# Performance work log

Hardware: AMD Instinct MI355X
Metric: run time of the kernel (lower is better)

The kernel has to match this reference:

```python
import jax, jax.numpy as jnp
import numpy as np

N_NODES = 100000
N_EDGES = 1600000
HIDDEN = 48
LAYERS = 4
ALPHA = 0.1
THETA = 0.5


def setup_inputs() -> dict:
    key = jax.random.key(0)
    ks = jax.random.split(key, 6)
    x = jax.random.normal(ks[0], (N_NODES, 3), dtype=jnp.float32)
    edge_index = jax.random.randint(ks[1], (2, N_EDGES), 0, N_NODES, dtype=jnp.int32)
    W0 = jax.random.normal(ks[2], (3, HIDDEN), dtype=jnp.float32) * 0.3
    b0 = jnp.zeros((HIDDEN,), dtype=jnp.float32)
    convW = jax.random.normal(ks[3], (LAYERS, HIDDEN, HIDDEN), dtype=jnp.float32) * (1.0 / np.sqrt(HIDDEN))
    W1 = jax.random.normal(ks[4], (HIDDEN, HIDDEN), dtype=jnp.float32) * (1.0 / np.sqrt(HIDDEN))
    b1 = jnp.zeros((HIDDEN,), dtype=jnp.float32)
    return {"x": x, "edge_index": edge_index, "W0": W0, "b0": b0,
            "convW": convW, "W1": W1, "b1": b1}


def reference(x, edge_index, W0, b0, convW, W1, b1):
    # lin0 + relu; x0 is the initial residual (dropout=0 / eval mode -> identity)
    h = jax.nn.relu(x @ W0 + b0)
    x0 = h
    src, dst = edge_index[0], edge_index[1]
    n = h.shape[0]
    for l in range(LAYERS):
        # sparse propagation: A @ h via gather + segment_sum (unit edge weights, normalize=False)
        agg = jax.ops.segment_sum(h[src], dst, num_segments=n)
        beta = float(np.log(THETA / (l + 1) + 1.0))
        # GCNII shared-weights branch: t = (1-alpha)*Ah + alpha*x0; out = (1-beta)*t + beta*(t @ W)
        t = (1.0 - ALPHA) * agg + ALPHA * x0
        h = jax.nn.relu((1.0 - beta) * t + beta * (t @ convW[l]))
    out = h @ W1 + b1
    return jax.nn.log_softmax(out, axis=-1)
```

## Files before the change

### kernel.cpp

```cpp
#include <hip/hip_runtime.h>
#include <math.h>

#define N_NODES 100000
#define N_EDGES 1600000
#define HID 48
#define HPAD 64
#define ALPHA 0.1f

#define LBLK 6250
#define NPW 4

typedef unsigned short u16;
typedef unsigned int u32;

__device__ __forceinline__ float bf_lo(u32 u) { return __uint_as_float(u << 16); }
__device__ __forceinline__ float bf_hi(u32 u) { return __uint_as_float(u & 0xffff0000u); }
__device__ __forceinline__ u16 f2bf(float f) {
    u32 b = __float_as_uint(f);
    b += 0x7fff + ((b >> 16) & 1);
    return (u16)(b >> 16);
}
__device__ __forceinline__ u32 pack2(float a, float b) {
    return (u32)f2bf(a) | ((u32)f2bf(b) << 16);
}

#define RLANE(x, l) __int_as_float(__builtin_amdgcn_readlane(__float_as_int(x), (l)))

__global__ __launch_bounds__(256) void lin0_k(const float* __restrict__ x, const float* __restrict__ W0,
                                              const float* __restrict__ b0, u16* __restrict__ h0) {
    int t = blockIdx.x * 256 + threadIdx.x;
    if (t >= N_NODES * 6) return;
    int node = t / 6, oct = t % 6;
    float xv0 = x[node * 3 + 0], xv1 = x[node * 3 + 1], xv2 = x[node * 3 + 2];
    float v[8];
#pragma unroll
    for (int j = 0; j < 8; j++) {
        int f = oct * 8 + j;
        float s = b0[f] + xv0 * W0[0 * HID + f] + xv1 * W0[1 * HID + f] + xv2 * W0[2 * HID + f];
        v[j] = s > 0.f ? s : 0.f;
    }
    uint4 p;
    p.x = pack2(v[0], v[1]); p.y = pack2(v[2], v[3]);
    p.z = pack2(v[4], v[5]); p.w = pack2(v[6], v[7]);
    *(uint4*)(h0 + (size_t)node * HPAD + oct * 8) = p;
}

__global__ __launch_bounds__(256) void count_k(const int* __restrict__ dst, int* __restrict__ deg,
                                               int* __restrict__ rank) {
    int e = blockIdx.x * 256 + threadIdx.x;
    if (e < N_EDGES) rank[e] = atomicAdd(&deg[dst[e]], 1);
}

__global__ __launch_bounds__(256) void scan1_k(const int* __restrict__ deg, int* __restrict__ rowptr,
                                               int* __restrict__ partial) {
    __shared__ int sums[256];
    int tid = threadIdx.x;
    int base = blockIdx.x * 2048 + tid * 8;
    int v[8]; int s = 0;
#pragma unroll
    for (int j = 0; j < 8; j++) { int idx = base + j; v[j] = (idx < N_NODES) ? deg[idx] : 0; s += v[j]; }
    sums[tid] = s; __syncthreads();
    for (int off = 1; off < 256; off <<= 1) {
        int t = (tid >= off) ? sums[tid - off] : 0;
        __syncthreads();
        sums[tid] += t;
        __syncthreads();
    }
    if (tid == 255) partial[blockIdx.x] = sums[255];
    int run = (tid > 0) ? sums[tid - 1] : 0;
#pragma unroll
    for (int j = 0; j < 8; j++) { int idx = base + j; if (idx < N_NODES) rowptr[idx] = run; run += v[j]; }
}

__global__ void scan2_k(int* __restrict__ partial, int* __restrict__ rowptr, int nblk) {
    int lane = threadIdx.x & 63;
    int v = (lane < nblk) ? partial[lane] : 0;
    for (int off = 1; off < 64; off <<= 1) {
        int t = __shfl_up(v, off);
        if (lane >= off) v += t;
    }
    int excl = __shfl_up(v, 1);
    if (lane == 0) excl = 0;
    if (lane < nblk) partial[lane] = excl;
    if (lane == 63) rowptr[N_NODES] = v;
}

__global__ __launch_bounds__(256) void scan3_k(int* __restrict__ rowptr, const int* __restrict__ partial) {
    int tid = threadIdx.x;
    int base = blockIdx.x * 2048 + tid * 8;
    int add = partial[blockIdx.x];
#pragma unroll
    for (int j = 0; j < 8; j++) {
        int idx = base + j;
        if (idx < N_NODES) rowptr[idx] += add;
    }
}

__global__ __launch_bounds__(256) void bucket_k(const int* __restrict__ src, const int* __restrict__ dst,
                                                const int* __restrict__ rank, const int* __restrict__ rowptr,
                                                int* __restrict__ ssrc) {
    int e = blockIdx.x * 256 + threadIdx.x;
    if (e < N_EDGES) {
        int d = dst[e];
        ssrc[rowptr[d] + rank[e]] = src[e];
    }
}

__global__ __launch_bounds__(256) void layer_k(const u16* __restrict__ h_in, const u16* __restrict__ x0,
                                               const int* __restrict__ rowptr, const int* __restrict__ ssrc,
                                               const float* __restrict__ W, float beta,
                                               u16* __restrict__ h_out) {
    __shared__ float sM[2304];
    int tid = threadIdx.x, lane = tid & 63;
    for (int i = tid; i < 2304; i += 256) {
        int r = i / 48, c = i - r * 48;
        float v = beta * W[i];
        if (r == c) v += 1.f - beta;
        sM[i] = v;
    }
    __syncthreads();
    int f = lane < 48 ? lane : 0;
    float wreg[48];
#pragma unroll
    for (int r = 0; r < 48; ++r) wreg[r] = sM[r * 48 + f];

    int chunk = lane & 7;
    int slot  = lane >> 3;
    int cc = chunk < 6 ? chunk : 0;
    int wid = blockIdx.x * 4 + (tid >> 6);

    for (int i = 0; i < NPW; ++i) {
        int node = wid * NPW + i;
        if (node >= N_NODES) break;
        int e0 = rowptr[node], e1 = rowptr[node + 1];
        float a0 = 0.f, a1 = 0.f, a2 = 0.f, a3 = 0.f, a4 = 0.f, a5 = 0.f, a6 = 0.f, a7 = 0.f;
        int e = e0;
        for (; e + 16 <= e1; e += 16) {
            int sA = ssrc[e + slot];
            int sB = ssrc[e + 8 + slot];
            const uint4 wA = *(const uint4*)(h_in + ((size_t)sA << 6) + cc * 8);
            const uint4 wB = *(const uint4*)(h_in + ((size_t)sB << 6) + cc * 8);
            a0 += bf_lo(wA.x) + bf_lo(wB.x);
            a1 += bf_hi(wA.x) + bf_hi(wB.x);
            a2 += bf_lo(wA.y) + bf_lo(wB.y);
            a3 += bf_hi(wA.y) + bf_hi(wB.y);
            a4 += bf_lo(wA.z) + bf_lo(wB.z);
            a5 += bf_hi(wA.z) + bf_hi(wB.z);
            a6 += bf_lo(wA.w) + bf_lo(wB.w);
            a7 += bf_hi(wA.w) + bf_hi(wB.w);
        }
        for (; e < e1; e += 8) {
            int idx = e + slot;
            int s = ssrc[idx < e1 ? idx : e];
            const uint4 w = *(const uint4*)(h_in + ((size_t)s << 6) + cc * 8);
            if (idx < e1) {
                a0 += bf_lo(w.x); a1 += bf_hi(w.x);
                a2 += bf_lo(w.y); a3 += bf_hi(w.y);
                a4 += bf_lo(w.z); a5 += bf_hi(w.z);
                a6 += bf_lo(w.w); a7 += bf_hi(w.w);
            }
        }
#pragma unroll
        for (int off = 8; off <= 32; off <<= 1) {
            a0 += __shfl_xor(a0, off); a1 += __shfl_xor(a1, off);
            a2 += __shfl_xor(a2, off); a3 += __shfl_xor(a3, off);
            a4 += __shfl_xor(a4, off); a5 += __shfl_xor(a5, off);
            a6 += __shfl_xor(a6, off); a7 += __shfl_xor(a7, off);
        }
        const uint4 xv = *(const uint4*)(x0 + ((size_t)node << 6) + cc * 8);
        a0 = (1.f - ALPHA) * a0 + ALPHA * bf_lo(xv.x);
        a1 = (1.f - ALPHA) * a1 + ALPHA * bf_hi(xv.x);
        a2 = (1.f - ALPHA) * a2 + ALPHA * bf_lo(xv.y);
        a3 = (1.f - ALPHA) * a3 + ALPHA * bf_hi(xv.y);
        a4 = (1.f - ALPHA) * a4 + ALPHA * bf_lo(xv.z);
        a5 = (1.f - ALPHA) * a5 + ALPHA * bf_hi(xv.z);
        a6 = (1.f - ALPHA) * a6 + ALPHA * bf_lo(xv.w);
        a7 = (1.f - ALPHA) * a7 + ALPHA * bf_hi(xv.w);
        float p0 = 0.f, p1 = 0.f, p2 = 0.f, p3 = 0.f;
#pragma unroll
        for (int c = 0; c < 6; ++c) {
            p0 = fmaf(RLANE(a0, c), wreg[c * 8 + 0], p0);
            p1 = fmaf(RLANE(a1, c), wreg[c * 8 + 1], p1);
            p2 = fmaf(RLANE(a2, c), wreg[c * 8 + 2], p2);
            p3 = fmaf(RLANE(a3, c), wreg[c * 8 + 3], p3);
            p0 = fmaf(RLANE(a4, c), wreg[c * 8 + 4], p0);
            p1 = fmaf(RLANE(a5, c), wreg[c * 8 + 5], p1);
            p2 = fmaf(RLANE(a6, c), wreg[c * 8 + 6], p2);
            p3 = fmaf(RLANE(a7, c), wreg[c * 8 + 7], p3);
        }
        float o = (p0 + p1) + (p2 + p3);
        if (lane < 48) h_out[((size_t)node << 6) + lane] = f2bf(o > 0.f ? o : 0.f);
    }
}

__global__ __launch_bounds__(256) void final_k(const u16* __restrict__ h, const float* __restrict__ W1,
                                               const float* __restrict__ b1, float* __restrict__ out) {
    __shared__ float sW[2304];
    int tid = threadIdx.x, lane = tid & 63;
    for (int i = tid; i < 2304; i += 256) sW[i] = W1[i];
    __syncthreads();
    int f = lane < 48 ? lane : 0;
    float wreg[48];
#pragma unroll
    for (int r = 0; r < 48; ++r) wreg[r] = sW[r * 48 + f];
    float bv = b1[f];
    int chunk = lane & 7;
    int cc = chunk < 6 ? chunk : 0;
    int wid = blockIdx.x * 4 + (tid >> 6);

    for (int i = 0; i < NPW; ++i) {
        int node = wid * NPW + i;
        if (node >= N_NODES) break;
        const uint4 hv = *(const uint4*)(h + ((size_t)node << 6) + cc * 8);
        float a0 = bf_lo(hv.x), a1 = bf_hi(hv.x), a2 = bf_lo(hv.y), a3 = bf_hi(hv.y);
        float a4 = bf_lo(hv.z), a5 = bf_hi(hv.z), a6 = bf_lo(hv.w), a7 = bf_hi(hv.w);
        float p0 = bv, p1 = 0.f, p2 = 0.f, p3 = 0.f;
#pragma unroll
        for (int c = 0; c < 6; ++c) {
            p0 = fmaf(RLANE(a0, c), wreg[c * 8 + 0], p0);
            p1 = fmaf(RLANE(a1, c), wreg[c * 8 + 1], p1);
            p2 = fmaf(RLANE(a2, c), wreg[c * 8 + 2], p2);
            p3 = fmaf(RLANE(a3, c), wreg[c * 8 + 3], p3);
            p0 = fmaf(RLANE(a4, c), wreg[c * 8 + 4], p0);
            p1 = fmaf(RLANE(a5, c), wreg[c * 8 + 5], p1);
            p2 = fmaf(RLANE(a6, c), wreg[c * 8 + 6], p2);
            p3 = fmaf(RLANE(a7, c), wreg[c * 8 + 7], p3);
        }
        float v = (lane < 48) ? (p0 + p1) + (p2 + p3) : -INFINITY;
        float m = v;
        for (int off = 32; off >= 1; off >>= 1) m = fmaxf(m, __shfl_xor(m, off));
        float ex = (lane < 48) ? expf(v - m) : 0.f;
        float sum = ex;
        for (int off = 32; off >= 1; off >>= 1) sum += __shfl_xor(sum, off);
        if (lane < 48) out[(size_t)node * 48 + lane] = v - m - logf(sum);
    }
}

extern "C" void kernel_launch(void* const* d_in, const int* in_sizes, int n_in,
                              void* d_out, int out_size, void* d_ws, size_t ws_size,
                              hipStream_t stream) {
    const float* x     = (const float*)d_in[0];
    const int*   ei    = (const int*)d_in[1];
    const float* W0    = (const float*)d_in[2];
    const float* b0    = (const float*)d_in[3];
    const float* convW = (const float*)d_in[4];
    const float* W1    = (const float*)d_in[5];
    const float* b1    = (const float*)d_in[6];
    float* out = (float*)d_out;
    const int* src = ei;
    const int* dst = ei + N_EDGES;

    char* ws = (char*)d_ws;
    size_t off = 0;
    u16* h0 = (u16*)(ws + off); off += (size_t)N_NODES * HPAD * 2;
    u16* hA = (u16*)(ws + off); off += (size_t)N_NODES * HPAD * 2;
    u16* hB = (u16*)(ws + off); off += (size_t)N_NODES * HPAD * 2;
    int* rank = (int*)hA;
    int* ssrc = (int*)(ws + off);   off += (size_t)N_EDGES * 4;
    int* rowptr = (int*)(ws + off); off += (size_t)(N_NODES + 1) * 4;
    off = (off + 255) & ~(size_t)255;
    int* deg = (int*)(ws + off);    off += (size_t)N_NODES * 4;
    off = (off + 255) & ~(size_t)255;
    int* partial = (int*)(ws + off); off += 64 * 4;

    hipMemsetAsync(deg, 0, (size_t)N_NODES * 4, stream);

    lin0_k<<<(N_NODES * 6 + 255) / 256, 256, 0, stream>>>(x, W0, b0, h0);
    count_k<<<6250, 256, 0, stream>>>(dst, deg, rank);
    scan1_k<<<49, 256, 0, stream>>>(deg, rowptr, partial);
    scan2_k<<<1, 64, 0, stream>>>(partial, rowptr, 49);
    scan3_k<<<49, 256, 0, stream>>>(rowptr, partial);
    bucket_k<<<6250, 256, 0, stream>>>(src, dst, rank, rowptr, ssrc);

    const float betas[4] = { logf(1.5f), logf(1.25f), logf(7.f / 6.f), logf(1.125f) };

    layer_k<<<LBLK, 256, 0, stream>>>(h0, h0, rowptr, ssrc, convW + 0 * 2304, betas[0], hB);
    layer_k<<<LBLK, 256, 0, stream>>>(hB, h0, rowptr, ssrc, convW + 1 * 2304, betas[1], hA);
    layer_k<<<LBLK, 256, 0, stream>>>(hA, h0, rowptr, ssrc, convW + 2 * 2304, betas[2], hB);
    layer_k<<<LBLK, 256, 0, stream>>>(hB, h0, rowptr, ssrc, convW + 3 * 2304, betas[3], hA);
    final_k<<<LBLK, 256, 0, stream>>>(hA, W1, b1, out);
}
```

Baseline: 507.4 us.

## Software-pipeline neighbor gathers across nodes in layer kernel

Restructures the per-warp node loop into an explicit prefetch pipeline. The row pointers and the first 24 neighbor rows of the next node are loaded before the current node is reduced and transformed, so gather latency overlaps compute. Edges beyond the prefetched window fall back to a tail loop of 8 at a time. The bounds check on node is dropped, which relies on N_NODES being an exact multiple of the nodes per block. Keeping three uint4 prefetches per node live raises register pressure and may lower occupancy.

```diff
diff --git a/kernel.cpp b/kernel.cpp
--- a/kernel.cpp
+++ b/kernel.cpp
@@ -104,6 +104,79 @@
         int d = dst[e];
         ssrc[rowptr[d] + rank[e]] = src[e];
     }
+}
+
+struct PF { int e0, e1; uint4 wA, wB, wC; };
+
+__device__ __forceinline__ PF pf_load(const u16* __restrict__ h_in, const int* __restrict__ rowptr,
+                                      const int* __restrict__ ssrc, int node, int slot, int cc) {
+    PF p;
+    p.e0 = rowptr[node];
+    p.e1 = rowptr[node + 1];
+    int es = p.e0 < N_EDGES ? p.e0 : N_EDGES - 1;
+    int iA = p.e0 + slot, iB = p.e0 + 8 + slot, iC = p.e0 + 16 + slot;
+    int sA = ssrc[iA < p.e1 ? iA : es];
+    int sB = ssrc[iB < p.e1 ? iB : es];
+    int sC = ssrc[iC < p.e1 ? iC : es];
+    p.wA = *(const uint4*)(h_in + ((size_t)sA << 6) + cc * 8);
+    p.wB = *(const uint4*)(h_in + ((size_t)sB << 6) + cc * 8);
+    p.wC = *(const uint4*)(h_in + ((size_t)sC << 6) + cc * 8);
+    return p;
+}
+
+__device__ __forceinline__ void acc8(float& a0, float& a1, float& a2, float& a3,
+                                     float& a4, float& a5, float& a6, float& a7, const uint4& w) {
+    a0 += bf_lo(w.x); a1 += bf_hi(w.x);
+    a2 += bf_lo(w.y); a3 += bf_hi(w.y);
+    a4 += bf_lo(w.z); a5 += bf_hi(w.z);
+    a6 += bf_lo(w.w); a7 += bf_hi(w.w);
+}
+
+__device__ __forceinline__ void process_node(const PF& p, int node, int slot, int cc, int lane,
+                                             const float (&wreg)[48],
+                                             const u16* __restrict__ h_in, const u16* __restrict__ x0,
+                                             const int* __restrict__ ssrc, u16* __restrict__ h_out) {
+    const uint4 xv = *(const uint4*)(x0 + ((size_t)node << 6) + cc * 8);
+    float a0 = 0.f, a1 = 0.f, a2 = 0.f, a3 = 0.f, a4 = 0.f, a5 = 0.f, a6 = 0.f, a7 = 0.f;
+    int e0 = p.e0, e1 = p.e1;
+    if (e0 + slot < e1)      acc8(a0, a1, a2, a3, a4, a5, a6, a7, p.wA);
+    if (e0 + 8 + slot < e1)  acc8(a0, a1, a2, a3, a4, a5, a6, a7, p.wB);
+    if (e0 + 16 + slot < e1) acc8(a0, a1, a2, a3, a4, a5, a6, a7, p.wC);
+    for (int e = e0 + 24; e < e1; e += 8) {
+        int idx = e + slot;
+        int s = ssrc[idx < e1 ? idx : e];
+        const uint4 w = *(const uint4*)(h_in + ((size_t)s << 6) + cc * 8);
+        if (idx < e1) acc8(a0, a1, a2, a3, a4, a5, a6, a7, w);
+    }
+#pragma unroll
+    for (int off = 8; off <= 32; off <<= 1) {
+        a0 += __shfl_xor(a0, off); a1 += __shfl_xor(a1, off);
+        a2 += __shfl_xor(a2, off); a3 += __shfl_xor(a3, off);
+        a4 += __shfl_xor(a4, off); a5 += __shfl_xor(a5, off);
+        a6 += __shfl_xor(a6, off); a7 += __shfl_xor(a7, off);
+    }
+    a0 = (1.f - ALPHA) * a0 + ALPHA * bf_lo(xv.x);
+    a1 = (1.f - ALPHA) * a1 + ALPHA * bf_hi(xv.x);
+    a2 = (1.f - ALPHA) * a2 + ALPHA * bf_lo(xv.y);
+    a3 = (1.f - ALPHA) * a3 + ALPHA * bf_hi(xv.y);
+    a4 = (1.f - ALPHA) * a4 + ALPHA * bf_lo(xv.z);
+    a5 = (1.f - ALPHA) * a5 + ALPHA * bf_hi(xv.z);
+    a6 = (1.f - ALPHA) * a6 + ALPHA * bf_lo(xv.w);
+    a7 = (1.f - ALPHA) * a7 + ALPHA * bf_hi(xv.w);
+    float p0 = 0.f, p1 = 0.f, p2 = 0.f, p3 = 0.f;
+#pragma unroll
+    for (int c = 0; c < 6; ++c) {
+        p0 = fmaf(RLANE(a0, c), wreg[c * 8 + 0], p0);
+        p1 = fmaf(RLANE(a1, c), wreg[c * 8 + 1], p1);
+        p2 = fmaf(RLANE(a2, c), wreg[c * 8 + 2], p2);
+        p3 = fmaf(RLANE(a3, c), wreg[c * 8 + 3], p3);
+        p0 = fmaf(RLANE(a4, c), wreg[c * 8 + 4], p0);
+        p1 = fmaf(RLANE(a5, c), wreg[c * 8 + 5], p1);
+        p2 = fmaf(RLANE(a6, c), wreg[c * 8 + 6], p2);
+        p3 = fmaf(RLANE(a7, c), wreg[c * 8 + 7], p3);
+    }
+    float o = (p0 + p1) + (p2 + p3);
+    if (lane < 48) h_out[((size_t)node << 6) + lane] = f2bf(o > 0.f ? o : 0.f);
 }
 
 __global__ __launch_bounds__(256) void layer_k(const u16* __restrict__ h_in, const u16* __restrict__ x0,
@@ -127,70 +200,17 @@
     int chunk = lane & 7;
     int slot  = lane >> 3;
     int cc = chunk < 6 ? chunk : 0;
-    int wid = blockIdx.x * 4 + (tid >> 6);
-
-    for (int i = 0; i < NPW; ++i) {
-        int node = wid * NPW + i;
-        if (node >= N_NODES) break;
-        int e0 = rowptr[node], e1 = rowptr[node + 1];
-        float a0 = 0.f, a1 = 0.f, a2 = 0.f, a3 = 0.f, a4 = 0.f, a5 = 0.f, a6 = 0.f, a7 = 0.f;
-        int e = e0;
-        for (; e + 16 <= e1; e += 16) {
-            int sA = ssrc[e + slot];
-            int sB = ssrc[e + 8 + slot];
-            const uint4 wA = *(const uint4*)(h_in + ((size_t)sA << 6) + cc * 8);
-            const uint4 wB = *(const uint4*)(h_in + ((size_t)sB << 6) + cc * 8);
-            a0 += bf_lo(wA.x) + bf_lo(wB.x);
-            a1 += bf_hi(wA.x) + bf_hi(wB.x);
-            a2 += bf_lo(wA.y) + bf_lo(wB.y);
-            a3 += bf_hi(wA.y) + bf_hi(wB.y);
-            a4 += bf_lo(wA.z) + bf_lo(wB.z);
-            a5 += bf_hi(wA.z) + bf_hi(wB.z);
-            a6 += bf_lo(wA.w) + bf_lo(wB.w);
-            a7 += bf_hi(wA.w) + bf_hi(wB.w);
-        }
-        for (; e < e1; e += 8) {
-            int idx = e + slot;
-            int s = ssrc[idx < e1 ? idx : e];
-            const uint4 w = *(const uint4*)(h_in + ((size_t)s << 6) + cc * 8);
-            if (idx < e1) {
-                a0 += bf_lo(w.x); a1 += bf_hi(w.x);
-                a2 += bf_lo(w.y); a3 += bf_hi(w.y);
-                a4 += bf_lo(w.z); a5 += bf_hi(w.z);
-                a6 += bf_lo(w.w); a7 += bf_hi(w.w);
-            }
-        }
-#pragma unroll
-        for (int off = 8; off <= 32; off <<= 1) {
-            a0 += __shfl_xor(a0, off); a1 += __shfl_xor(a1, off);
-            a2 += __shfl_xor(a2, off); a3 += __shfl_xor(a3, off);
-            a4 += __shfl_xor(a4, off); a5 += __shfl_xor(a5, off);
-            a6 += __shfl_xor(a6, off); a7 += __shfl_xor(a7, off);
-        }
-        const uint4 xv = *(const uint4*)(x0 + ((size_t)node << 6) + cc * 8);
-        a0 = (1.f - ALPHA) * a0 + ALPHA * bf_lo(xv.x);
-        a1 = (1.f - ALPHA) * a1 + ALPHA * bf_hi(xv.x);
-        a2 = (1.f - ALPHA) * a2 + ALPHA * bf_lo(xv.y);
-        a3 = (1.f - ALPHA) * a3 + ALPHA * bf_hi(xv.y);
-        a4 = (1.f - ALPHA) * a4 + ALPHA * bf_lo(xv.z);
-        a5 = (1.f - ALPHA) * a5 + ALPHA * bf_hi(xv.z);
-        a6 = (1.f - ALPHA) * a6 + ALPHA * bf_lo(xv.w);
-        a7 = (1.f - ALPHA) * a7 + ALPHA * bf_hi(xv.w);
-        float p0 = 0.f, p1 = 0.f, p2 = 0.f, p3 = 0.f;
-#pragma unroll
-        for (int c = 0; c < 6; ++c) {
-            p0 = fmaf(RLANE(a0, c), wreg[c * 8 + 0], p0);
-            p1 = fmaf(RLANE(a1, c), wreg[c * 8 + 1], p1);
-            p2 = fmaf(RLANE(a2, c), wreg[c * 8 + 2], p2);
-            p3 = fmaf(RLANE(a3, c), wreg[c * 8 + 3], p3);
-            p0 = fmaf(RLANE(a4, c), wreg[c * 8 + 4], p0);
-            p1 = fmaf(RLANE(a5, c), wreg[c * 8 + 5], p1);
-            p2 = fmaf(RLANE(a6, c), wreg[c * 8 + 6], p2);
-            p3 = fmaf(RLANE(a7, c), wreg[c * 8 + 7], p3);
-        }
-        float o = (p0 + p1) + (p2 + p3);
-        if (lane < 48) h_out[((size_t)node << 6) + lane] = f2bf(o > 0.f ? o : 0.f);
-    }
+    int wid = __builtin_amdgcn_readfirstlane(blockIdx.x * 4 + (tid >> 6));
+    int base = wid * NPW;
+
+    PF pA = pf_load(h_in, rowptr, ssrc, base + 0, slot, cc);
+    PF pB = pf_load(h_in, rowptr, ssrc, base + 1, slot, cc);
+    process_node(pA, base + 0, slot, cc, lane, wreg, h_in, x0, ssrc, h_out);
+    PF pC = pf_load(h_in, rowptr, ssrc, base + 2, slot, cc);
+    process_node(pB, base + 1, slot, cc, lane, wreg, h_in, x0, ssrc, h_out);
+    PF pD = pf_load(h_in, rowptr, ssrc, base + 3, slot, cc);
+    process_node(pC, base + 2, slot, cc, lane, wreg, h_in, x0, ssrc, h_out);
+    process_node(pD, base + 3, slot, cc, lane, wreg, h_in, x0, ssrc, h_out);
 }
 
 __global__ __launch_bounds__(256) void final_k(const u16* __restrict__ h, const float* __restrict__ W1,
```

Result: faster. 445.6 us (-12.2%).
